# Performance work log

Measured on AMD Instinct MI355X. Metric: run time of the kernel, lower is better.

The kernel has to match this reference:

```python
import jax, jax.numpy as jnp
import numpy as np

N, C, H, W = 8, 16, 512, 512
GRID = 8                     # 8x8 grid of 64x64 blocks => components
K = GRID * GRID + 1          # label 0 = background, 1..64 = components


def setup_inputs() -> dict:
    key = jax.random.key(0)
    k1, k2 = jax.random.split(key)
    color = jax.random.normal(k1, (N, C, H, W), dtype=jnp.float32)
    # blocky ground-truth probability map so connected components == blocks
    bh = H // GRID
    block_vals = jax.random.uniform(k2, (N, GRID, GRID), dtype=jnp.float32)
    gt = jnp.repeat(jnp.repeat(block_vals, bh, axis=1), bh, axis=2)[:, None, :, :]
    # per-pixel component label: block id (1..64) where gt>0.5, else 0
    block_ids = (jnp.arange(GRID)[:, None] * GRID + jnp.arange(GRID)[None, :] + 1).astype(jnp.int32)
    block_ids_full = jnp.repeat(jnp.repeat(block_ids, bh, axis=0), bh, axis=1)
    block_ids_full = jnp.broadcast_to(block_ids_full[None], (N, H, W))
    labels = jnp.where(gt[:, 0] > 0.5, block_ids_full, 0)
    return {"color": color, "gt": gt, "labels": labels}


def reference(color, gt, labels):
    lambda_inter, margin, thr, min_pixels, eps = 0.4, 0.5, 0.5, 20.0, 1e-6
    Nb, Cc, Hh, Ww = color.shape
    Kc = K
    sub = (gt[:, 0] > thr).astype(color.dtype)      # (N,H,W)
    bg = 1.0 - sub
    bg_cnt = bg.sum(axis=(1, 2))                    # (N,)
    # background masked mean per image: (N,C)
    m_bg = jnp.einsum('nchw,nhw->nc', color, bg) / (bg_cnt + eps)[:, None]
    # per-component segment reductions (single pass over pixels)
    feat = color.transpose(0, 2, 3, 1).reshape(-1, Cc)          # (N*H*W, C)
    seg = (labels + jnp.arange(Nb, dtype=labels.dtype)[:, None, None] * Kc).reshape(-1)
    counts = jax.ops.segment_sum(jnp.ones(seg.shape[0], color.dtype), seg, Nb * Kc).reshape(Nb, Kc)
    fsum = jax.ops.segment_sum(feat, seg, Nb * Kc).reshape(Nb, Kc, Cc)
    sqsum = jax.ops.segment_sum((feat * feat).sum(-1), seg, Nb * Kc).reshape(Nb, Kc)
    denom = counts + eps
    m_sub = fsum / denom[..., None]                 # (N,K,C)
    # intra: sum_{p in comp} ||f_p - m_sub||^2 / (count+eps), expanded form
    intra = (sqsum - 2.0 * (m_sub * fsum).sum(-1) + counts * (m_sub * m_sub).sum(-1)) / denom
    dist = jnp.sqrt(((m_sub - m_bg[:, None, :]) ** 2).sum(-1) + 1e-12)
    inter = jnp.maximum(margin - dist, 0.0) ** 2
    valid = (counts >= min_pixels) & (jnp.arange(Kc)[None, :] > 0) & (bg_cnt[:, None] >= min_pixels)
    v = valid.astype(color.dtype)
    total = v.sum()
    safe_total = jnp.maximum(total, 1.0)
    intra_avg = (intra * v).sum() / safe_total
    inter_avg = (inter * v).sum() / safe_total
    loss = jnp.where(total > 0, intra_avg + lambda_inter * inter_avg, 0.0)
    return loss
```

## Files before the change

kernel.cpp:

```cpp
#include <hip/hip_runtime.h>


namespace {
constexpr int NIMG = 8;
constexpr int NCH  = 16;
constexpr int HWPX = 512 * 512;
constexpr int KSEG = 65;
constexpr int NF   = 18;
constexpr int SPANS = HWPX / 64;
constexpr int TABF  = NIMG * KSEG * NF;
constexpr int WS_TAB = NIMG * SPANS;
constexpr float EPSV   = 1e-6f;
constexpr float MARGIN = 0.5f;
constexpr float LAMBDA = 0.4f;
constexpr float MINPIX = 20.0f;
typedef float fx4 __attribute__((ext_vector_type(4)));
}

__global__ __launch_bounds__(256) void spanlab_kernel(
    const int* __restrict__ labels, int* __restrict__ spanlab,
    float* __restrict__ tab)
{
    const int n   = blockIdx.y;
    const int tid = threadIdx.x;
    const int grp = tid >> 4, l16 = tid & 15, wgrp = (tid & 63) >> 4;
    const int span = blockIdx.x * 16 + grp;
    const int p    = span * 64 + l16 * 4;

    if (n == 0 && tid < 37) {
        const int idx = blockIdx.x * 37 + tid;
        if (idx < TABF) tab[idx] = 0.0f;
    }

    const int4 lab = *reinterpret_cast<const int4*>(labels + (size_t)n * HWPX + p);
    const int  lab0 = __shfl(lab.x, 0, 16);
    const bool uni  = (lab.x == lab.y) && (lab.x == lab.z) &&
                      (lab.x == lab.w) && (lab.x == lab0);
    const unsigned long long b = __ballot((int)uni);
    const unsigned long long m = 0xFFFFull << (wgrp * 16);
    if (l16 == 0)
        spanlab[n * SPANS + span] = ((b & m) == m) ? lab0 : -1;
}

__global__ __launch_bounds__(256) void accum_kernel(
    const float* __restrict__ color,
    const int*   __restrict__ labels,
    const int*   __restrict__ spanlab,
    float* __restrict__ tab)
{
    __shared__ float ltab[KSEG * NF];
    const int tid = threadIdx.x;
    for (int i = tid; i < KSEG * NF; i += 256) ltab[i] = 0.0f;
    __syncthreads();

    const int n = blockIdx.y;
    const float* colN = color  + (size_t)n * NCH * HWPX;
    const int*   labN = labels + (size_t)n * HWPX;
    const int*   slN  = spanlab + n * SPANS;

    const int grp = tid >> 4;
    const int l16 = tid & 15;

    const int stride = gridDim.x * 1024;
    for (int base = blockIdx.x * 1024; base < HWPX; base += stride) {
        const int span = (base >> 6) + grp;
        const int p    = base + grp * 64 + l16 * 4;
        const int slab = slN[span];

        if (slab >= 0) {
            float fs[NCH];
            float sq = 0.0f;
            #pragma unroll
            for (int c = 0; c < NCH; ++c) {
                const fx4 v = __builtin_nontemporal_load(
                    reinterpret_cast<const fx4*>(colN + (size_t)c * HWPX + p));
                fs[c] = (v.x + v.y) + (v.z + v.w);
                sq += v.x * v.x + v.y * v.y + v.z * v.z + v.w * v.w;
            }
            #pragma unroll
            for (int c = 0; c < 8; ++c) {
                const float snd = (l16 & 8) ? fs[c] : fs[c + 8];
                const float kp  = (l16 & 8) ? fs[c + 8] : fs[c];
                fs[c] = kp + __shfl_xor(snd, 8, 16);
            }
            #pragma unroll
            for (int c = 0; c < 4; ++c) {
                const float snd = (l16 & 4) ? fs[c] : fs[c + 4];
                const float kp  = (l16 & 4) ? fs[c + 4] : fs[c];
                fs[c] = kp + __shfl_xor(snd, 4, 16);
            }
            #pragma unroll
            for (int c = 0; c < 2; ++c) {
                const float snd = (l16 & 2) ? fs[c] : fs[c + 2];
                const float kp  = (l16 & 2) ? fs[c + 2] : fs[c];
                fs[c] = kp + __shfl_xor(snd, 2, 16);
            }
            {
                const float snd = (l16 & 1) ? fs[0] : fs[1];
                const float kp  = (l16 & 1) ? fs[1] : fs[0];
                fs[0] = kp + __shfl_xor(snd, 1, 16);
            }
            sq += __shfl_xor(sq, 8, 16);
            sq += __shfl_xor(sq, 4, 16);
            sq += __shfl_xor(sq, 2, 16);
            sq += __shfl_xor(sq, 1, 16);

            float* seg = ltab + slab * NF;
            atomicAdd(seg + 2 + l16, fs[0]);
            if (l16 == 0) {
                atomicAdd(seg + 0, 64.0f);
                atomicAdd(seg + 1, sq);
            }
        } else {
            const int4 lb = *reinterpret_cast<const int4*>(labN + p);
            const int labv[4] = {lb.x, lb.y, lb.z, lb.w};
            for (int i = 0; i < 4; ++i) {
                float sqp = 0.0f;
                float* seg = ltab + labv[i] * NF;
                for (int c = 0; c < NCH; ++c) {
                    const float x = colN[(size_t)c * HWPX + p + i];
                    sqp += x * x;
                    atomicAdd(seg + 2 + c, x);
                }
                atomicAdd(seg + 0, 1.0f);
                atomicAdd(seg + 1, sqp);
            }
        }
    }

    __syncthreads();
    float* tabN = tab + (size_t)n * KSEG * NF;
    for (int i = tid; i < KSEG * NF; i += 256) {
        const float x = ltab[i];
        if (x != 0.0f) atomicAdd(tabN + i, x);
    }
}

__global__ __launch_bounds__(256) void finalize_kernel(
    const float* __restrict__ tab, float* __restrict__ out)
{
    __shared__ float mbg[NIMG][NCH];
    __shared__ float bgcnt[NIMG];
    __shared__ float r0[256], r1[256], r2[256];
    const int tid = threadIdx.x;
    if (tid < NIMG * NCH) {
        const int n = tid / NCH, c = tid % NCH;
        const float* b = tab + (size_t)n * KSEG * NF;
        const float cnt = b[0];
        mbg[n][c] = b[2 + c] / (cnt + EPSV);
        if (c == 0) bgcnt[n] = cnt;
    }
    __syncthreads();

    float vsum = 0.0f, intraS = 0.0f, interS = 0.0f;
    for (int idx = tid; idx < NIMG * KSEG; idx += 256) {
        const int n = idx / KSEG, k = idx % KSEG;
        if (k == 0) continue;
        const float* s = tab + ((size_t)n * KSEG + k) * NF;
        const float cnt = s[0], sq = s[1];
        const float denom = cnt + EPSV;
        float d2 = 0.0f, msf = 0.0f, msm = 0.0f;
        #pragma unroll
        for (int c = 0; c < NCH; ++c) {
            const float f  = s[2 + c];
            const float mu = f / denom;
            msf += mu * f;
            msm += mu * mu;
            const float dd = mu - mbg[n][c];
            d2 += dd * dd;
        }
        const float intra = (sq - 2.0f * msf + cnt * msm) / denom;
        const float dist  = sqrtf(d2 + 1e-12f);
        const float t     = fmaxf(MARGIN - dist, 0.0f);
        const float inter = t * t;
        if ((cnt >= MINPIX) && (bgcnt[n] >= MINPIX)) {
            vsum += 1.0f; intraS += intra; interS += inter;
        }
    }
    r0[tid] = vsum; r1[tid] = intraS; r2[tid] = interS;
    __syncthreads();
    for (int sft = 128; sft; sft >>= 1) {
        if (tid < sft) {
            r0[tid] += r0[tid + sft];
            r1[tid] += r1[tid + sft];
            r2[tid] += r2[tid + sft];
        }
        __syncthreads();
    }
    if (tid == 0) {
        const float total = r0[0];
        const float safe  = fmaxf(total, 1.0f);
        out[0] = (total > 0.0f) ? (r1[0] + LAMBDA * r2[0]) / safe : 0.0f;
    }
}

extern "C" void kernel_launch(void* const* d_in, const int* in_sizes, int n_in,
                              void* d_out, int out_size, void* d_ws, size_t ws_size,
                              hipStream_t stream) {
    const float* color  = (const float*)d_in[0];
    const int*   labels = (const int*)d_in[2];
    float* ws  = (float*)d_ws;
    float* out = (float*)d_out;

    int*   spanlab = (int*)ws;
    float* tab     = ws + WS_TAB;

    dim3 gridA(SPANS / 16, NIMG);
    spanlab_kernel<<<gridA, 256, 0, stream>>>(labels, spanlab, tab);

    dim3 gridB(128, NIMG);
    accum_kernel<<<gridB, 256, 0, stream>>>(color, labels, spanlab, tab);

    finalize_kernel<<<1, 256, 0, stream>>>(tab, out);
}
```

Baseline: 38.08 us.

## Split channels across two 16-lane groups per span and double accum grid

Each 64-pixel span is now handled by two 16-thread groups, each loading and reducing half of the channels. This halves per-thread register use and load depth and raises in-flight parallelism; the accumulation grid is doubled to match. Nontemporal loads are replaced by plain float4 loads. The cost is more shared-memory atomics on the squared-sum field, which each half now adds separately, and a redundant label check per half.

```diff
diff --git a/kernel.cpp b/kernel.cpp
--- a/kernel.cpp
+++ b/kernel.cpp
@@ -14,7 +14,6 @@
 constexpr float MARGIN = 0.5f;
 constexpr float LAMBDA = 0.4f;
 constexpr float MINPIX = 20.0f;
-typedef float fx4 __attribute__((ext_vector_type(4)));
 }
 
 __global__ __launch_bounds__(256) void spanlab_kernel(
@@ -60,56 +59,53 @@
 
     const int grp = tid >> 4;
     const int l16 = tid & 15;
-
-    const int stride = gridDim.x * 1024;
-    for (int base = blockIdx.x * 1024; base < HWPX; base += stride) {
-        const int span = (base >> 6) + grp;
-        const int p    = base + grp * 64 + l16 * 4;
+    const int h   = grp & 1;
+    const int cb  = h * 8;
+
+    for (int sbase = blockIdx.x * 8; sbase < SPANS; sbase += gridDim.x * 8) {
+        const int span = sbase + (grp >> 1);
+        const int p    = span * 64 + l16 * 4;
         const int slab = slN[span];
 
         if (slab >= 0) {
-            float fs[NCH];
+            float fs[8];
             float sq = 0.0f;
             #pragma unroll
-            for (int c = 0; c < NCH; ++c) {
-                const fx4 v = __builtin_nontemporal_load(
-                    reinterpret_cast<const fx4*>(colN + (size_t)c * HWPX + p));
+            for (int c = 0; c < 8; ++c) {
+                const float4 v = *reinterpret_cast<const float4*>(
+                    colN + (size_t)(cb + c) * HWPX + p);
                 fs[c] = (v.x + v.y) + (v.z + v.w);
                 sq += v.x * v.x + v.y * v.y + v.z * v.z + v.w * v.w;
             }
             #pragma unroll
-            for (int c = 0; c < 8; ++c) {
-                const float snd = (l16 & 8) ? fs[c] : fs[c + 8];
-                const float kp  = (l16 & 8) ? fs[c + 8] : fs[c];
+            for (int c = 0; c < 4; ++c) {
+                const float kp  = (l16 & 8) ? fs[c + 4] : fs[c];
+                const float snd = (l16 & 8) ? fs[c] : fs[c + 4];
                 fs[c] = kp + __shfl_xor(snd, 8, 16);
-            }
-            #pragma unroll
-            for (int c = 0; c < 4; ++c) {
-                const float snd = (l16 & 4) ? fs[c] : fs[c + 4];
-                const float kp  = (l16 & 4) ? fs[c + 4] : fs[c];
-                fs[c] = kp + __shfl_xor(snd, 4, 16);
             }
             #pragma unroll
             for (int c = 0; c < 2; ++c) {
-                const float snd = (l16 & 2) ? fs[c] : fs[c + 2];
-                const float kp  = (l16 & 2) ? fs[c + 2] : fs[c];
-                fs[c] = kp + __shfl_xor(snd, 2, 16);
+                const float kp  = (l16 & 4) ? fs[c + 2] : fs[c];
+                const float snd = (l16 & 4) ? fs[c] : fs[c + 2];
+                fs[c] = kp + __shfl_xor(snd, 4, 16);
             }
             {
-                const float snd = (l16 & 1) ? fs[0] : fs[1];
-                const float kp  = (l16 & 1) ? fs[1] : fs[0];
-                fs[0] = kp + __shfl_xor(snd, 1, 16);
-            }
+                const float kp  = (l16 & 2) ? fs[1] : fs[0];
+                const float snd = (l16 & 2) ? fs[0] : fs[1];
+                fs[0] = kp + __shfl_xor(snd, 2, 16);
+            }
+            fs[0] += __shfl_xor(fs[0], 1, 16);
             sq += __shfl_xor(sq, 8, 16);
             sq += __shfl_xor(sq, 4, 16);
             sq += __shfl_xor(sq, 2, 16);
             sq += __shfl_xor(sq, 1, 16);
 
             float* seg = ltab + slab * NF;
-            atomicAdd(seg + 2 + l16, fs[0]);
+            if ((l16 & 1) == 0)
+                atomicAdd(seg + 2 + cb + ((l16 >> 1) & 7), fs[0]);
             if (l16 == 0) {
-                atomicAdd(seg + 0, 64.0f);
                 atomicAdd(seg + 1, sq);
+                if (h == 0) atomicAdd(seg + 0, 64.0f);
             }
         } else {
             const int4 lb = *reinterpret_cast<const int4*>(labN + p);
@@ -117,13 +113,13 @@
             for (int i = 0; i < 4; ++i) {
                 float sqp = 0.0f;
                 float* seg = ltab + labv[i] * NF;
-                for (int c = 0; c < NCH; ++c) {
-                    const float x = colN[(size_t)c * HWPX + p + i];
+                for (int c = 0; c < 8; ++c) {
+                    const float x = colN[(size_t)(cb + c) * HWPX + p + i];
                     sqp += x * x;
-                    atomicAdd(seg + 2 + c, x);
+                    atomicAdd(seg + 2 + cb + c, x);
                 }
-                atomicAdd(seg + 0, 1.0f);
                 atomicAdd(seg + 1, sqp);
+                if (h == 0) atomicAdd(seg + 0, 1.0f);
             }
         }
     }
@@ -208,7 +204,7 @@
     dim3 gridA(SPANS / 16, NIMG);
     spanlab_kernel<<<gridA, 256, 0, stream>>>(labels, spanlab, tab);
 
-    dim3 gridB(128, NIMG);
+    dim3 gridB(256, NIMG);
     accum_kernel<<<gridB, 256, 0, stream>>>(color, labels, spanlab, tab);
 
     finalize_kernel<<<1, 256, 0, stream>>>(tab, out);
```

Result: faster. 37.32 us (-2.0%).
